# Optimization experiments

Measured on AMD Instinct MI355X. Metric: run time of the kernel, lower is better.

The kernel has to match this reference:

```python
import jax, jax.numpy as jnp
import numpy as np

N_NODES = 100000
N_EDGES = 3200000
N_FEAT = 512
N_CLASS = 40
HIDDEN = 16


def _agnn(x, src, dst, beta, num_nodes):
    # PyG AGNNConv: cosine-similarity attention, softmax over incoming edges.
    norm = jnp.linalg.norm(x, axis=1, keepdims=True)
    x_norm = x / jnp.maximum(norm, 1e-12)
    # per-edge logits: beta * <x_norm_dst, x_norm_src>
    alpha = beta * jnp.sum(x_norm[dst] * x_norm[src], axis=1)  # [E]
    # segment softmax over destination nodes
    m = jax.ops.segment_max(alpha, dst, num_segments=num_nodes)  # [N]
    e = jnp.exp(alpha - m[dst])
    s = jax.ops.segment_sum(e, dst, num_segments=num_nodes)  # [N]
    w = e / jnp.maximum(s[dst], 1e-16)  # [E]
    # weighted aggregation of source features to destination
    return jax.ops.segment_sum(x[src] * w[:, None], dst, num_segments=num_nodes)


def setup_inputs() -> dict:
    key = jax.random.key(0)
    ks = jax.random.split(key, 7)
    x = jax.random.normal(ks[0], (N_NODES, N_FEAT), dtype=jnp.float32)
    edge_index = jax.random.randint(ks[1], (2, N_EDGES), 0, N_NODES, dtype=jnp.int32)
    lin1_w = jax.random.normal(ks[2], (HIDDEN, N_FEAT), dtype=jnp.float32) * (1.0 / np.sqrt(N_FEAT))
    lin1_b = jax.random.normal(ks[3], (HIDDEN,), dtype=jnp.float32) * 0.01
    beta2 = jnp.ones((1,), dtype=jnp.float32)
    lin2_w = jax.random.normal(ks[4], (N_CLASS, HIDDEN), dtype=jnp.float32) * (1.0 / np.sqrt(HIDDEN))
    lin2_b = jax.random.normal(ks[5], (N_CLASS,), dtype=jnp.float32) * 0.01
    return {"x": x, "edge_index": edge_index, "lin1_w": lin1_w, "lin1_b": lin1_b,
            "beta2": beta2, "lin2_w": lin2_w, "lin2_b": lin2_b}


def reference(x, edge_index, lin1_w, lin1_b, beta2, lin2_w, lin2_b):
    src, dst = edge_index[0], edge_index[1]
    n = x.shape[0]
    # eval mode: dropout is identity
    h = jax.nn.relu(x @ lin1_w.T + lin1_b)          # [N, 16]
    h = _agnn(h, src, dst, jnp.float32(1.0), n)     # prop1: beta fixed at 1
    h = _agnn(h, src, dst, beta2[0], n)             # prop2: learnable beta
    logits = h @ lin2_w.T + lin2_b                  # [N, C]
    return jax.nn.log_softmax(logits, axis=1)
```

## Files before the change

### kernel.cpp

```cpp
#include <hip/hip_runtime.h>

#define N_NODES 100000
#define N_EDGES 3200000
#define N_FEAT  512
#define HID     16
#define N_CLASS 40

#define BSHIFT  9
#define BMASK   ((1 << BSHIFT) - 1)
#define NB      196
#define CAP     18432
#define EPB     4096

#define BIN_BLOCKS  ((N_EDGES + EPB - 1) / EPB)
#define NT          (N_NODES / 16)
#define LIN1_BLOCKS ((NT + 3) / 4)

typedef __attribute__((ext_vector_type(8))) short bf16x8;
typedef __attribute__((ext_vector_type(4))) float f32x4;

__device__ inline short2 split_bf(float v) {
    const unsigned u = __float_as_uint(v);
    const short hi = (short)(u >> 16);
    const float hf = __uint_as_float(u & 0xFFFF0000u);
    const short lo = (short)(__float_as_uint(v - hf) >> 16);
    return make_short2(hi, lo);
}
__device__ inline unsigned short f2bf_rtn(float v) {
    unsigned u = __float_as_uint(v);
    u += 0x7FFFu + ((u >> 16) & 1u);
    return (unsigned short)(u >> 16);
}
__device__ inline float bf2f(unsigned short u) {
    return __uint_as_float(((unsigned)u) << 16);
}

struct BinSmem {
    int hist[NB]; int lofs[NB]; int base[NB]; int rk[NB];
    int buf[256]; int stage[EPB]; unsigned short sbkt[EPB];
};
struct Lin1Smem { short bfH[16 * 64 * 8]; short bfL[16 * 64 * 8]; };

__device__ void bin_body(char* smemraw,
                         const int* __restrict__ src,
                         const int* __restrict__ dst,
                         int* __restrict__ cursor,
                         int* __restrict__ binned) {
    BinSmem& sm = *(BinSmem*)smemraw;
    const int t = threadIdx.x;
    for (int i = t; i < NB; i += 256) { sm.hist[i] = 0; sm.rk[i] = 0; }
    __syncthreads();

    const int e0 = blockIdx.x * EPB;
    int bk[EPB / 256];
    int vv[EPB / 256];
#pragma unroll
    for (int k = 0; k < EPB / 256; k++) {
        const int e = e0 + k * 256 + t;
        if (e < N_EDGES) {
            const int d = dst[e], s = src[e];
            bk[k] = d >> BSHIFT;
            vv[k] = (s << BSHIFT) | (d & BMASK);
            atomicAdd(&sm.hist[bk[k]], 1);
        } else bk[k] = -1;
    }
    __syncthreads();

    {
        const int v = (t < NB) ? sm.hist[t] : 0;
        sm.buf[t] = v; __syncthreads();
        for (int o = 1; o < 256; o <<= 1) {
            const int a = (t >= o) ? sm.buf[t - o] : 0;
            __syncthreads();
            sm.buf[t] += a;
            __syncthreads();
        }
        if (t < NB) sm.lofs[t] = sm.buf[t] - v;
    }
    if (t < NB && sm.hist[t] > 0)
        sm.base[t] = t * CAP + atomicAdd(&cursor[t], sm.hist[t]);

#pragma unroll
    for (int k = 0; k < EPB / 256; k++) {
        if (bk[k] >= 0) {
            const int r = atomicAdd(&sm.rk[bk[k]], 1);
            const int slot = sm.lofs[bk[k]] + r;
            sm.stage[slot] = vv[k];
            sm.sbkt[slot] = (unsigned short)bk[k];
        }
    }
    __syncthreads();

    const int nloc = min(EPB, N_EDGES - e0);
    for (int s2 = t; s2 < nloc; s2 += 256) {
        const int b = sm.sbkt[s2];
        binned[sm.base[b] + (s2 - sm.lofs[b])] = sm.stage[s2];
    }
}

__device__ void lin1_body(char* smemraw, int lblk,
                          const float* __restrict__ x,
                          const float* __restrict__ w1,
                          const float* __restrict__ b1,
                          unsigned short* __restrict__ xnb,
                          float* __restrict__ normv) {
    Lin1Smem& sm = *(Lin1Smem*)smemraw;
    const int t = threadIdx.x;
    for (int f = t; f < 16 * 64; f += 256) {
        const int kt  = f >> 6;
        const int ln  = f & 63;
        const int col = ln & 15;
        const int k0  = kt * 32 + (ln >> 4) * 8;
        const float4 v0 = *(const float4*)(w1 + col * N_FEAT + k0);
        const float4 v1 = *(const float4*)(w1 + col * N_FEAT + k0 + 4);
        bf16x8 hh, ll;
        short2 r;
        r = split_bf(v0.x); hh[0] = r.x; ll[0] = r.y;
        r = split_bf(v0.y); hh[1] = r.x; ll[1] = r.y;
        r = split_bf(v0.z); hh[2] = r.x; ll[2] = r.y;
        r = split_bf(v0.w); hh[3] = r.x; ll[3] = r.y;
        r = split_bf(v1.x); hh[4] = r.x; ll[4] = r.y;
        r = split_bf(v1.y); hh[5] = r.x; ll[5] = r.y;
        r = split_bf(v1.z); hh[6] = r.x; ll[6] = r.y;
        r = split_bf(v1.w); hh[7] = r.x; ll[7] = r.y;
        ((bf16x8*)sm.bfH)[f] = hh;
        ((bf16x8*)sm.bfL)[f] = ll;
    }
    __syncthreads();

    const int wv   = t >> 6;
    const int l    = t & 63;
    const int tile = lblk * 4 + wv;
    if (tile >= NT) return;

    const int r0 = tile * 16;
    const float* xp = x + (size_t)(r0 + (l & 15)) * N_FEAT + ((l >> 4) * 8);

    f32x4 acc = {0.f, 0.f, 0.f, 0.f};
    float4 c0 = *(const float4*)(xp);
    float4 c1 = *(const float4*)(xp + 4);
#pragma unroll
    for (int kt = 0; kt < 16; ++kt) {
        float4 n0, n1;
        if (kt < 15) {
            n0 = *(const float4*)(xp + (kt + 1) * 32);
            n1 = *(const float4*)(xp + (kt + 1) * 32 + 4);
        }
        bf16x8 ah, al;
        short2 r;
        r = split_bf(c0.x); ah[0] = r.x; al[0] = r.y;
        r = split_bf(c0.y); ah[1] = r.x; al[1] = r.y;
        r = split_bf(c0.z); ah[2] = r.x; al[2] = r.y;
        r = split_bf(c0.w); ah[3] = r.x; al[3] = r.y;
        r = split_bf(c1.x); ah[4] = r.x; al[4] = r.y;
        r = split_bf(c1.y); ah[5] = r.x; al[5] = r.y;
        r = split_bf(c1.z); ah[6] = r.x; al[6] = r.y;
        r = split_bf(c1.w); ah[7] = r.x; al[7] = r.y;
        const bf16x8 bh = ((const bf16x8*)sm.bfH)[kt * 64 + l];
        const bf16x8 bl = ((const bf16x8*)sm.bfL)[kt * 64 + l];
        acc = __builtin_amdgcn_mfma_f32_16x16x32_bf16(ah, bh, acc, 0, 0, 0);
        acc = __builtin_amdgcn_mfma_f32_16x16x32_bf16(al, bh, acc, 0, 0, 0);
        acc = __builtin_amdgcn_mfma_f32_16x16x32_bf16(ah, bl, acc, 0, 0, 0);
        c0 = n0; c1 = n1;
    }

    const float bias = b1[l & 15];
#pragma unroll
    for (int r = 0; r < 4; ++r) {
        const float v = fmaxf(acc[r] + bias, 0.f);
        float ss = v * v;
        ss += __shfl_xor(ss, 1); ss += __shfl_xor(ss, 2);
        ss += __shfl_xor(ss, 4); ss += __shfl_xor(ss, 8);
        const float nrm = sqrtf(ss);
        const float rn  = 1.f / fmaxf(nrm, 1e-12f);
        const int row = r0 + (l >> 4) * 4 + r;
        xnb[(size_t)row * HID + (l & 15)] = f2bf_rtn(v * rn);
        if ((l & 15) == 0) normv[row] = nrm;
    }
}

__global__ __launch_bounds__(256) void k_bin_lin1(const int* __restrict__ src,
                                                  const int* __restrict__ dst,
                                                  int* __restrict__ cursor,
                                                  int* __restrict__ binned,
                                                  const float* __restrict__ x,
                                                  const float* __restrict__ w1,
                                                  const float* __restrict__ b1,
                                                  unsigned short* __restrict__ xnb,
                                                  float* __restrict__ normv) {
    __shared__ __align__(16) char smem[sizeof(Lin1Smem) > sizeof(BinSmem)
                                       ? sizeof(Lin1Smem) : sizeof(BinSmem)];
    if (blockIdx.x < BIN_BLOCKS)
        bin_body(smem, src, dst, cursor, binned);
    else
        lin1_body(smem, blockIdx.x - BIN_BLOCKS, x, w1, b1, xnb, normv);
}

__global__ __launch_bounds__(512) void k_csr(const int* __restrict__ cursor,
                                             int* __restrict__ binned,
                                             int* __restrict__ row_start,
                                             unsigned short* __restrict__ row_cnt) {
    __shared__ int cnts[512];
    __shared__ int cur[512];
    __shared__ int buf[512];
    __shared__ int lcsr[CAP];

    const int t = threadIdx.x;
    const int b = blockIdx.x;
    const int s0 = b * CAP;
    const int n = cursor[b];

    cnts[t] = 0;
    __syncthreads();
    for (int i = t; i < n; i += 512)
        atomicAdd(&cnts[binned[s0 + i] & BMASK], 1);
    __syncthreads();

    {
        const int v = cnts[t];
        buf[t] = v; __syncthreads();
        for (int o = 1; o < 512; o <<= 1) {
            const int a = (t >= o) ? buf[t - o] : 0;
            __syncthreads();
            buf[t] += a;
            __syncthreads();
        }
        cur[t] = buf[t] - v;
        const int node = (b << BSHIFT) + t;
        if (node < N_NODES) {
            row_start[node] = s0 + cur[t];
            row_cnt[node]   = (unsigned short)v;
        }
    }
    __syncthreads();

    for (int i = t; i < n; i += 512) {
        const int v = binned[s0 + i];
        const int p = atomicAdd(&cur[v & BMASK], 1);
        lcsr[p] = v >> BSHIFT;
    }
    __syncthreads();

    for (int i = t; i < n; i += 512) binned[s0 + i] = lcsr[i];
}

template <int LAST>
__global__ __launch_bounds__(256) void k_agnn(const int* __restrict__ row_start,
                                              const unsigned short* __restrict__ row_cnt,
                                              const int* __restrict__ csr_src,
                                              const unsigned short* __restrict__ xnb,
                                              const float* __restrict__ normv,
                                              const float* __restrict__ betap,
                                              const float* __restrict__ w2,
                                              const float* __restrict__ b2,
                                              float* __restrict__ out,
                                              unsigned short* __restrict__ outb,
                                              float* __restrict__ out_norm) {
    __shared__ float w2s[N_CLASS][HID + 1];
    __shared__ float b2s[N_CLASS];
    if (LAST) {
        for (int i = threadIdx.x; i < N_CLASS * HID; i += 256)
            w2s[i / HID][i % HID] = w2[i];
        if (threadIdx.x < N_CLASS) b2s[threadIdx.x] = b2[threadIdx.x];
        __syncthreads();
    }

    const int l16  = threadIdx.x & 15;
    const int node = (blockIdx.x * 256 + threadIdx.x) >> 4;
    const float beta  = betap ? betap[0] : 1.0f;
    const float shift = fabsf(beta);

    const int rs  = row_start[node];
    const int cnt = row_cnt[node];

    const bf16x8* xd = (const bf16x8*)(xnb + (size_t)node * HID);
    const bf16x8 dlo = xd[0], dhi = xd[1];
    float dd[16];
#pragma unroll
    for (int i = 0; i < 8; i++) {
        dd[i]     = bf2f((unsigned short)dlo[i]);
        dd[i + 8] = bf2f((unsigned short)dhi[i]);
    }

    float acc[16];
#pragma unroll
    for (int i = 0; i < 16; i++) acc[i] = 0.f;
    float swl = 0.f;

    bool ok = (l16 < cnt);
    int sidx = ok ? csr_src[rs + l16] : 0;
    const bf16x8* xs0 = (const bf16x8*)(xnb + (size_t)sidx * HID);
    bf16x8 slo = xs0[0], shi = xs0[1];
    float nj = normv[sidx];

    for (int t = 0; t < cnt; t += 16) {
        const int k2 = t + 16 + l16;
        const bool ok2 = (k2 < cnt);
        const int sidx2 = ok2 ? csr_src[rs + k2] : 0;
        const bf16x8* xs2 = (const bf16x8*)(xnb + (size_t)sidx2 * HID);
        const bf16x8 slo2 = xs2[0], shi2 = xs2[1];
        const float nj2 = normv[sidx2];

        float sr[16];
#pragma unroll
        for (int i = 0; i < 8; i++) {
            sr[i]     = bf2f((unsigned short)slo[i]);
            sr[i + 8] = bf2f((unsigned short)shi[i]);
        }
        float p0 = 0.f, p1 = 0.f, p2 = 0.f, p3 = 0.f;
#pragma unroll
        for (int i = 0; i < 4; i++) {
            p0 += sr[i]      * dd[i];
            p1 += sr[i + 4]  * dd[i + 4];
            p2 += sr[i + 8]  * dd[i + 8];
            p3 += sr[i + 12] * dd[i + 12];
        }
        const float dot = (p0 + p1) + (p2 + p3);
        const float w = ok ? __expf(beta * dot - shift) : 0.f;
        swl += w;
        const float wn = w * nj;
#pragma unroll
        for (int i = 0; i < 16; i++) acc[i] += wn * sr[i];

        sidx = sidx2; slo = slo2; shi = shi2; nj = nj2; ok = ok2;
    }

#pragma unroll
    for (int m = 1; m < 16; m <<= 1) {
#pragma unroll
        for (int r = 0; r < 16; r += 2 * m) {
            const float sel  = (l16 & m) ? acc[r] : acc[r + m];
            const float got  = __shfl_xor(sel, m);
            const float mine = (l16 & m) ? acc[r + m] : acc[r];
            acc[r] = mine + got;
        }
    }
    float sw = swl;
    sw += __shfl_xor(sw, 1); sw += __shfl_xor(sw, 2);
    sw += __shfl_xor(sw, 4); sw += __shfl_xor(sw, 8);

    const float v = acc[0] / fmaxf(sw, 1e-16f);

    if (!LAST) {
        float ss = v * v;
        ss += __shfl_xor(ss, 1); ss += __shfl_xor(ss, 2);
        ss += __shfl_xor(ss, 4); ss += __shfl_xor(ss, 8);
        const float nrm = sqrtf(ss);
        const float rn  = 1.f / fmaxf(nrm, 1e-12f);
        outb[(size_t)node * HID + l16] = f2bf_rtn(v * rn);
        if (l16 == 0) out_norm[node] = nrm;
    } else {
        float vv[16];
#pragma unroll
        for (int k = 0; k < 16; k++) vv[k] = __shfl(v, k, 16);
        const int c0 = l16, c1 = l16 + 16, c2 = l16 + 32;
        float lg0 = b2s[c0], lg1 = b2s[c1];
        float lg2 = (l16 < 8) ? b2s[c2] : -3.0e38f;
#pragma unroll
        for (int k = 0; k < 16; k++) {
            lg0 += vv[k] * w2s[c0][k];
            lg1 += vv[k] * w2s[c1][k];
            if (l16 < 8) lg2 += vv[k] * w2s[c2][k];
        }
        float m = fmaxf(lg0, lg1);
        if (l16 < 8) m = fmaxf(m, lg2);
        m = fmaxf(m, __shfl_xor(m, 1)); m = fmaxf(m, __shfl_xor(m, 2));
        m = fmaxf(m, __shfl_xor(m, 4)); m = fmaxf(m, __shfl_xor(m, 8));
        float s = __expf(lg0 - m) + __expf(lg1 - m)
                + ((l16 < 8) ? __expf(lg2 - m) : 0.f);
        s += __shfl_xor(s, 1); s += __shfl_xor(s, 2);
        s += __shfl_xor(s, 4); s += __shfl_xor(s, 8);
        const float lse = m + __logf(s);

        float* orow = out + (size_t)node * N_CLASS;
        orow[c0] = lg0 - lse;
        orow[c1] = lg1 - lse;
        if (l16 < 8) orow[c2] = lg2 - lse;
    }
}

extern "C" void kernel_launch(void* const* d_in, const int* in_sizes, int n_in,
                              void* d_out, int out_size, void* d_ws, size_t ws_size,
                              hipStream_t stream) {
    const float* x     = (const float*)d_in[0];
    const int*   ei    = (const int*)  d_in[1];
    const float* w1    = (const float*)d_in[2];
    const float* b1    = (const float*)d_in[3];
    const float* beta2 = (const float*)d_in[4];
    const float* w2    = (const float*)d_in[5];
    const float* b2    = (const float*)d_in[6];
    float* out = (float*)d_out;

    const int* srcp = ei;
    const int* dstp = ei + N_EDGES;

    unsigned short* xnb1 = (unsigned short*)d_ws;
    unsigned short* xnb2 = xnb1 + (size_t)N_NODES * HID;
    float* norm1 = (float*)(xnb2 + (size_t)N_NODES * HID);
    float* norm2 = norm1 + N_NODES;
    int* row_start = (int*)(norm2 + N_NODES);
    unsigned short* row_cnt = (unsigned short*)(row_start + N_NODES);
    int* cursor = (int*)(row_cnt + N_NODES + (N_NODES & 1));
    int* binned = cursor + NB + 2;

    const int agnnGrid = N_NODES * HID / 256;

    hipMemsetAsync(cursor, 0, NB * sizeof(int), stream);

    k_bin_lin1<<<BIN_BLOCKS + LIN1_BLOCKS, 256, 0, stream>>>(
        srcp, dstp, cursor, binned, x, w1, b1, xnb1, norm1);

    k_csr<<<NB, 512, 0, stream>>>(cursor, binned, row_start, row_cnt);

    k_agnn<0><<<agnnGrid, 256, 0, stream>>>(row_start, row_cnt, binned, xnb1,
                                            norm1, nullptr, nullptr, nullptr,
                                            nullptr, xnb2, norm2);
    k_agnn<1><<<agnnGrid, 256, 0, stream>>>(row_start, row_cnt, binned, xnb2,
                                            norm2, beta2, w2, b2,
                                            out, nullptr, nullptr);
}
```

Before: 200.0 us.

## Switch AGNN aggregation to one thread per node with LDS-staged CSR indices

The AGNN kernel now maps one thread to each node instead of a 16-lane group per node. Each thread walks its incoming edges serially and keeps all 16 features in registers. Each block stages its contiguous slice of CSR source indices into shared memory, and the 16-lane shuffle reductions for the aggregation, norm and log-softmax are removed. Output writes are vectorised. In exchange, all lanes of a wavefront loop up to the wavefront's maximum degree, so degree imbalance causes divergence. Each thread also does a 32-byte gather per edge without coalescing across lanes, and register pressure in the final layer rises with 40 logits per thread.

```diff
diff --git a/kernel.cpp b/kernel.cpp
--- a/kernel.cpp
+++ b/kernel.cpp
@@ -11,10 +11,11 @@
 #define NB      196
 #define CAP     18432
 #define EPB     4096
+#define EC_CAP  9216
 
 #define BIN_BLOCKS  ((N_EDGES + EPB - 1) / EPB)
-#define NT          (N_NODES / 16)
-#define LIN1_BLOCKS ((NT + 3) / 4)
+#define NT_TILES    (N_NODES / 16)
+#define LIN1_BLOCKS ((NT_TILES + 3) / 4)
 
 typedef __attribute__((ext_vector_type(8))) short bf16x8;
 typedef __attribute__((ext_vector_type(4))) float f32x4;
@@ -131,7 +132,7 @@
     const int wv   = t >> 6;
     const int l    = t & 63;
     const int tile = lblk * 4 + wv;
-    if (tile >= NT) return;
+    if (tile >= NT_TILES) return;
 
     const int r0 = tile * 16;
     const float* xp = x + (size_t)(r0 + (l & 15)) * N_FEAT + ((l >> 4) * 8);
@@ -256,24 +257,44 @@
                                               float* __restrict__ out,
                                               unsigned short* __restrict__ outb,
                                               float* __restrict__ out_norm) {
-    __shared__ float w2s[N_CLASS][HID + 1];
+    __shared__ int ldsCsr[EC_CAP];
+    __shared__ float w2s[HID][N_CLASS + 1];
     __shared__ float b2s[N_CLASS];
+    __shared__ int sRs0, sNE;
+
+    const int t256 = threadIdx.x;
+    const int node = blockIdx.x * 256 + t256;
+    const bool alive = node < N_NODES;
+
     if (LAST) {
-        for (int i = threadIdx.x; i < N_CLASS * HID; i += 256)
-            w2s[i / HID][i % HID] = w2[i];
-        if (threadIdx.x < N_CLASS) b2s[threadIdx.x] = b2[threadIdx.x];
-        __syncthreads();
-    }
-
-    const int l16  = threadIdx.x & 15;
-    const int node = (blockIdx.x * 256 + threadIdx.x) >> 4;
+        for (int i = t256; i < N_CLASS * HID; i += 256)
+            w2s[i % HID][i / HID] = w2[i];
+        if (t256 < N_CLASS) b2s[t256] = b2[t256];
+    }
+
+    const int rs  = alive ? row_start[node] : 0;
+    const int cnt = alive ? (int)row_cnt[node] : 0;
+
+    if (t256 == 0) {
+        const int base = blockIdx.x * 256;
+        const int last = min(base + 256, N_NODES) - 1;
+        const int r0 = row_start[base];
+        sRs0 = r0;
+        sNE  = row_start[last] + (int)row_cnt[last] - r0;
+    }
+    __syncthreads();
+    const int rs0 = sRs0;
+    const int nStage = min(sNE, EC_CAP);
+    for (int i = t256; i < nStage; i += 256)
+        ldsCsr[i] = csr_src[rs0 + i];
+    __syncthreads();
+
     const float beta  = betap ? betap[0] : 1.0f;
     const float shift = fabsf(beta);
-
-    const int rs  = row_start[node];
-    const int cnt = row_cnt[node];
-
-    const bf16x8* xd = (const bf16x8*)(xnb + (size_t)node * HID);
+    const int off = rs - rs0;
+
+    const int nodeSafe = alive ? node : 0;
+    const bf16x8* xd = (const bf16x8*)(xnb + (size_t)nodeSafe * HID);
     const bf16x8 dlo = xd[0], dhi = xd[1];
     float dd[16];
 #pragma unroll
@@ -282,21 +303,29 @@
         dd[i + 8] = bf2f((unsigned short)dhi[i]);
     }
 
+    int mcnt = cnt;
+#pragma unroll
+    for (int m = 1; m < 64; m <<= 1) mcnt = max(mcnt, __shfl_xor(mcnt, m));
+
     float acc[16];
 #pragma unroll
     for (int i = 0; i < 16; i++) acc[i] = 0.f;
     float swl = 0.f;
 
-    bool ok = (l16 < cnt);
-    int sidx = ok ? csr_src[rs + l16] : 0;
+    bool ok = (0 < cnt);
+    int sidx = 0;
+    if (ok) { const int p = off; sidx = (p < nStage) ? ldsCsr[p] : csr_src[rs]; }
     const bf16x8* xs0 = (const bf16x8*)(xnb + (size_t)sidx * HID);
     bf16x8 slo = xs0[0], shi = xs0[1];
     float nj = normv[sidx];
 
-    for (int t = 0; t < cnt; t += 16) {
-        const int k2 = t + 16 + l16;
-        const bool ok2 = (k2 < cnt);
-        const int sidx2 = ok2 ? csr_src[rs + k2] : 0;
+    for (int t = 0; t < mcnt; ++t) {
+        const bool ok2 = (t + 1 < cnt);
+        int sidx2 = 0;
+        if (ok2) {
+            const int p = off + t + 1;
+            sidx2 = (p < nStage) ? ldsCsr[p] : csr_src[rs + t + 1];
+        }
         const bf16x8* xs2 = (const bf16x8*)(xnb + (size_t)sidx2 * HID);
         const bf16x8 slo2 = xs2[0], shi2 = xs2[1];
         const float nj2 = normv[sidx2];
@@ -322,60 +351,60 @@
 #pragma unroll
         for (int i = 0; i < 16; i++) acc[i] += wn * sr[i];
 
-        sidx = sidx2; slo = slo2; shi = shi2; nj = nj2; ok = ok2;
-    }
-
-#pragma unroll
-    for (int m = 1; m < 16; m <<= 1) {
-#pragma unroll
-        for (int r = 0; r < 16; r += 2 * m) {
-            const float sel  = (l16 & m) ? acc[r] : acc[r + m];
-            const float got  = __shfl_xor(sel, m);
-            const float mine = (l16 & m) ? acc[r + m] : acc[r];
-            acc[r] = mine + got;
-        }
-    }
-    float sw = swl;
-    sw += __shfl_xor(sw, 1); sw += __shfl_xor(sw, 2);
-    sw += __shfl_xor(sw, 4); sw += __shfl_xor(sw, 8);
-
-    const float v = acc[0] / fmaxf(sw, 1e-16f);
+        slo = slo2; shi = shi2; nj = nj2; ok = ok2;
+    }
+
+    const float inv = 1.f / fmaxf(swl, 1e-16f);
+    float v[16];
+#pragma unroll
+    for (int i = 0; i < 16; i++) v[i] = acc[i] * inv;
 
     if (!LAST) {
-        float ss = v * v;
-        ss += __shfl_xor(ss, 1); ss += __shfl_xor(ss, 2);
-        ss += __shfl_xor(ss, 4); ss += __shfl_xor(ss, 8);
+        float ss = 0.f;
+#pragma unroll
+        for (int i = 0; i < 16; i++) ss += v[i] * v[i];
         const float nrm = sqrtf(ss);
         const float rn  = 1.f / fmaxf(nrm, 1e-12f);
-        outb[(size_t)node * HID + l16] = f2bf_rtn(v * rn);
-        if (l16 == 0) out_norm[node] = nrm;
+        if (alive) {
+            bf16x8 o0, o1;
+#pragma unroll
+            for (int i = 0; i < 8; i++) {
+                o0[i] = (short)f2bf_rtn(v[i] * rn);
+                o1[i] = (short)f2bf_rtn(v[i + 8] * rn);
+            }
+            bf16x8* orow = (bf16x8*)(outb + (size_t)node * HID);
+            orow[0] = o0; orow[1] = o1;
+            out_norm[node] = nrm;
+        }
     } else {
-        float vv[16];
-#pragma unroll
-        for (int k = 0; k < 16; k++) vv[k] = __shfl(v, k, 16);
-        const int c0 = l16, c1 = l16 + 16, c2 = l16 + 32;
-        float lg0 = b2s[c0], lg1 = b2s[c1];
-        float lg2 = (l16 < 8) ? b2s[c2] : -3.0e38f;
-#pragma unroll
-        for (int k = 0; k < 16; k++) {
-            lg0 += vv[k] * w2s[c0][k];
-            lg1 += vv[k] * w2s[c1][k];
-            if (l16 < 8) lg2 += vv[k] * w2s[c2][k];
-        }
-        float m = fmaxf(lg0, lg1);
-        if (l16 < 8) m = fmaxf(m, lg2);
-        m = fmaxf(m, __shfl_xor(m, 1)); m = fmaxf(m, __shfl_xor(m, 2));
-        m = fmaxf(m, __shfl_xor(m, 4)); m = fmaxf(m, __shfl_xor(m, 8));
-        float s = __expf(lg0 - m) + __expf(lg1 - m)
-                + ((l16 < 8) ? __expf(lg2 - m) : 0.f);
-        s += __shfl_xor(s, 1); s += __shfl_xor(s, 2);
-        s += __shfl_xor(s, 4); s += __shfl_xor(s, 8);
+        float lg[N_CLASS];
+#pragma unroll
+        for (int j = 0; j < N_CLASS; j++) lg[j] = b2s[j];
+#pragma unroll
+        for (int k = 0; k < HID; k++) {
+            const float vk = v[k];
+#pragma unroll
+            for (int j = 0; j < N_CLASS; j++) lg[j] += vk * w2s[k][j];
+        }
+        float m = -3.0e38f;
+#pragma unroll
+        for (int j = 0; j < N_CLASS; j++) m = fmaxf(m, lg[j]);
+        float s = 0.f;
+#pragma unroll
+        for (int j = 0; j < N_CLASS; j++) s += __expf(lg[j] - m);
         const float lse = m + __logf(s);
-
-        float* orow = out + (size_t)node * N_CLASS;
-        orow[c0] = lg0 - lse;
-        orow[c1] = lg1 - lse;
-        if (l16 < 8) orow[c2] = lg2 - lse;
+        if (alive) {
+            float4* orow = (float4*)(out + (size_t)node * N_CLASS);
+#pragma unroll
+            for (int q = 0; q < N_CLASS / 4; q++) {
+                float4 o;
+                o.x = lg[q * 4 + 0] - lse;
+                o.y = lg[q * 4 + 1] - lse;
+                o.z = lg[q * 4 + 2] - lse;
+                o.w = lg[q * 4 + 3] - lse;
+                orow[q] = o;
+            }
+        }
     }
 }
 
@@ -403,7 +432,7 @@
     int* cursor = (int*)(row_cnt + N_NODES + (N_NODES & 1));
     int* binned = cursor + NB + 2;
 
-    const int agnnGrid = N_NODES * HID / 256;
+    const int agnnGrid = (N_NODES + 255) / 256;
 
     hipMemsetAsync(cursor, 0, NB * sizeof(int), stream);
 
```

New measurement: 175.1 us. 12.4% less time.
